# Optimization experiments

Measured on AMD Instinct MI355X. Metric: run time of the kernel, lower is better.

Reference implementation:

```python
import jax, jax.numpy as jnp
import numpy as np

EPS = 0.05      # entropic regularization, matches eps arg in forward
ITERS = 100     # Sinkhorn fixed-point iterations (auction analog; converged math)

def setup_inputs() -> dict:
    key = jax.random.key(0)
    k1, k2 = jax.random.split(key)
    B, N, D = 16, 2048, 3
    x = jax.random.uniform(k1, (B, N, D), dtype=jnp.float32)
    y = jax.random.uniform(k2, (B, N, D), dtype=jnp.float32)
    return {"x": x, "y": y}

def _emd_mean(x, y):
    # pairwise squared distances: [B, N, N]
    x2 = jnp.sum(x * x, axis=-1)                      # [B, N]
    y2 = jnp.sum(y * y, axis=-1)                      # [B, N]
    xy = jnp.einsum('bnd,bmd->bnm', x, y)             # [B, N, N]
    C = x2[:, :, None] + y2[:, None, :] - 2.0 * xy
    C = jnp.maximum(C, 0.0)

    B, N, _ = C.shape
    logK = -C / EPS                                   # [B, N, N]
    log_mu = jnp.full((B, N), -jnp.log(jnp.float32(N)))
    log_nu = log_mu

    def body(carry, _):
        f, g = carry
        # f_i = eps*(log mu_i - logsumexp_j((g_j - C_ij)/eps))
        f = EPS * (log_mu - jax.nn.logsumexp(logK + (g / EPS)[:, None, :], axis=2))
        g = EPS * (log_nu - jax.nn.logsumexp(logK + (f / EPS)[:, :, None], axis=1))
        return (f, g), None

    f0 = jnp.zeros((B, N), dtype=C.dtype)
    g0 = jnp.zeros((B, N), dtype=C.dtype)
    (f, g), _ = jax.lax.scan(body, (f0, g0), None, length=ITERS)

    # transport plan P_ij = exp((f_i + g_j - C_ij)/eps) (already includes mu,nu)
    logP = (f[:, :, None] + g[:, None, :] - C) / EPS
    P = jnp.exp(logP)
    # per-source-point matched squared distance, scaled by N (row mass = 1/N)
    dis = jnp.sum(P * C, axis=2) * N                  # [B, N]
    return dis.mean()

def reference(x, y):
    return _emd_mean(x, y)
```

## Files before the change

### kernel.cpp

```cpp
#include <hip/hip_runtime.h>

#define BB 16
#define NN 2048
#define NITERS 100

#define K2E      28.853900817779268f
#define TWO_K2E  57.707801635558536f
#define INV2K    0.017328679513998632f
#define INV_K2E  0.034657359027997264f
#define INV4K    0.008664339756999316f
#define LMU      (-11.0f)

#if __has_builtin(__builtin_amdgcn_exp2f)
#define EXP2F(x) __builtin_amdgcn_exp2f(x)
#else
#define EXP2F(x) exp2f(x)
#endif

typedef float v2f __attribute__((ext_vector_type(2)));
typedef float v4f __attribute__((ext_vector_type(4)));

#define DSTORE(p, v) __hip_atomic_store((p), (v), __ATOMIC_RELAXED, __HIP_MEMORY_SCOPE_AGENT)
#define DLOAD(p)     __hip_atomic_load((p), __ATOMIC_RELAXED, __HIP_MEMORY_SCOPE_AGENT)

__device__ __forceinline__ float bfly8(const float acc[8], int lane) {
    const bool b0 = lane & 1, b1 = lane & 2, b2 = lane & 4;
    float v4[4], v2_[2], v1;
    #pragma unroll
    for (int i = 0; i < 4; ++i) {
        float recv = __shfl_xor(b0 ? acc[i] : acc[i+4], 1, 64);
        v4[i] = (b0 ? acc[i+4] : acc[i]) + recv;
    }
    #pragma unroll
    for (int i = 0; i < 2; ++i) {
        float recv = __shfl_xor(b1 ? v4[i] : v4[i+2], 2, 64);
        v2_[i] = (b1 ? v4[i+2] : v4[i]) + recv;
    }
    {
        float recv = __shfl_xor(b2 ? v2_[0] : v2_[1], 4, 64);
        v1 = (b2 ? v2_[1] : v2_[0]) + recv;
    }
    v1 += __shfl_xor(v1, 8, 64);
    v1 += __shfl_xor(v1, 16, 64);
    v1 += __shfl_xor(v1, 32, 64);
    return v1;
}

__device__ __forceinline__ float sumpassL(
    const v4f* __restrict__ U, const v4f* __restrict__ T,
    const float* __restrict__ sdv,
    int rloc, int jh, int lane, int w, float* pcomb)
{
    const int jb = (jh << 10) + lane;
    float dv[16];
    #pragma unroll
    for (int s = 0; s < 16; ++s)
        dv[s] = sdv[jb + (s << 6)];

    v2f xp0[4], xp1[4], xp2[4], acc2[4];
    #pragma unroll
    for (int p = 0; p < 4; ++p) {
        const v4f ua = U[rloc + 2*p];
        const v4f ub = U[rloc + 2*p + 1];
        xp0[p] = (v2f){ua.x * INV2K, ub.x * INV2K};
        xp1[p] = (v2f){ua.y * INV2K, ub.y * INV2K};
        xp2[p] = (v2f){ua.z * INV2K, ub.z * INV2K};
        acc2[p] = (v2f){0.f, 0.f};
    }
    #pragma unroll 4
    for (int s = 0; s < 16; ++s) {
        const v4f t = T[jb + (s << 6)];
        const float ad = dv[s];
        const v2f a0v = (v2f){t.x, t.x}, a1v = (v2f){t.y, t.y};
        const v2f a2v = (v2f){t.z, t.z}, adv = (v2f){ad, ad};
        #pragma unroll
        for (int qq = 0; qq < 4; ++qq) {
            v2f d = __builtin_elementwise_fma(xp0[qq], a0v,
                    __builtin_elementwise_fma(xp1[qq], a1v,
                    __builtin_elementwise_fma(xp2[qq], a2v, adv)));
            acc2[qq] += (v2f){EXP2F(d.x), EXP2F(d.y)};
        }
    }
    float acc[8];
    #pragma unroll
    for (int p = 0; p < 4; ++p) { acc[2*p] = acc2[p].x; acc[2*p+1] = acc2[p].y; }
    float v1 = bfly8(acc, lane);
    const int rr = ((lane & 1) << 2) | (lane & 2) | ((lane >> 2) & 1);
    if (lane < 8) pcomb[w * 8 + rr] = v1;
    __syncthreads();
    float Sc = 0.f;
    if (lane < 8) Sc = v1 + pcomb[(w ^ 1) * 8 + rr];
    return Sc;
}

__device__ __forceinline__ float sumpassA(
    const v4f* __restrict__ U, const v4f* __restrict__ T,
    const float* __restrict__ gd,
    int rloc, int jh, int lane, int w, float* pcomb)
{
    const int jb = (jh << 10) + lane;
    float dv[16];
    #pragma unroll
    for (int s = 0; s < 16; ++s)
        dv[s] = DLOAD(gd + jb + (s << 6));

    v2f xp0[4], xp1[4], xp2[4], acc2[4];
    #pragma unroll
    for (int p = 0; p < 4; ++p) {
        const v4f ua = U[rloc + 2*p];
        const v4f ub = U[rloc + 2*p + 1];
        xp0[p] = (v2f){ua.x * INV2K, ub.x * INV2K};
        xp1[p] = (v2f){ua.y * INV2K, ub.y * INV2K};
        xp2[p] = (v2f){ua.z * INV2K, ub.z * INV2K};
        acc2[p] = (v2f){0.f, 0.f};
    }
    #pragma unroll 4
    for (int s = 0; s < 16; ++s) {
        const v4f t = T[jb + (s << 6)];
        const float ad = dv[s];
        const v2f a0v = (v2f){t.x, t.x}, a1v = (v2f){t.y, t.y};
        const v2f a2v = (v2f){t.z, t.z}, adv = (v2f){ad, ad};
        #pragma unroll
        for (int qq = 0; qq < 4; ++qq) {
            v2f d = __builtin_elementwise_fma(xp0[qq], a0v,
                    __builtin_elementwise_fma(xp1[qq], a1v,
                    __builtin_elementwise_fma(xp2[qq], a2v, adv)));
            acc2[qq] += (v2f){EXP2F(d.x), EXP2F(d.y)};
        }
    }
    float acc[8];
    #pragma unroll
    for (int p = 0; p < 4; ++p) { acc[2*p] = acc2[p].x; acc[2*p+1] = acc2[p].y; }
    float v1 = bfly8(acc, lane);
    const int rr = ((lane & 1) << 2) | (lane & 2) | ((lane >> 2) & 1);
    if (lane < 8) pcomb[w * 8 + rr] = v1;
    __syncthreads();
    float Sc = 0.f;
    if (lane < 8) Sc = v1 + pcomb[(w ^ 1) * 8 + rr];
    return Sc;
}

__device__ __forceinline__ float epilA(
    const v4f* __restrict__ U, const v4f* __restrict__ T,
    const float* __restrict__ gB,
    float Aval, int rloc, int jh, int lane)
{
    const int jb = (jh << 10) + lane;
    float dv[16];
    #pragma unroll
    for (int s = 0; s < 16; ++s)
        dv[s] = DLOAD(gB + jb + (s << 6));

    float xr0[8], xr1[8], xr2[8], Ak[8], x2k[8];
    #pragma unroll
    for (int k = 0; k < 8; ++k) {
        const v4f u = U[rloc + k];
        xr0[k] = u.x * INV2K;
        xr1[k] = u.y * INV2K;
        xr2[k] = u.z * INV2K;
        const int src = ((k & 1) << 2) | (k & 2) | ((k >> 2) & 1);
        Ak[k]  = __shfl(Aval, src, 64);
        x2k[k] = K2E * (xr0[k]*xr0[k] + xr1[k]*xr1[k] + xr2[k]*xr2[k]);
    }
    float acc = 0.f;
    for (int s = 0; s < 16; ++s) {
        const v4f t = T[jb + (s << 6)];
        const float a0 = t.x, a1 = t.y, a2 = t.z, tb = dv[s];
        const float q2 = (a0*a0 + a1*a1 + a2*a2) * INV4K;
        #pragma unroll
        for (int k = 0; k < 8; ++k) {
            float d = fmaf(xr0[k], a0, fmaf(xr1[k], a1, fmaf(xr2[k], a2, tb)));
            float P = EXP2F(d + Ak[k]);
            float C = fmaxf((x2k[k] + q2 - (d - tb)) * INV_K2E, 0.f);
            acc = fmaf(P, C, acc);
        }
    }
    return acc;
}

__global__ __launch_bounds__(1024, 4) void emd_sinkhornT(
    const float* __restrict__ x, const float* __restrict__ y,
    float* __restrict__ Af, float* __restrict__ Bf,
    int* __restrict__ flags, float* __restrict__ out)
{
    extern __shared__ float S[];
    __shared__ float pcomb[16 * 8];
    __shared__ float wsum[16];

    const int tid  = threadIdx.x;
    const int lane = tid & 63;
    const int w    = tid >> 6;
    const int pr   = w >> 1;
    const int jh   = w & 1;
    const int blk  = blockIdx.x;
    const int b    = blk >> 4;
    const int q    = blk & 15;
    const int base = b * NN;
    const int row0 = q * 128;
    const int rlocA = row0 + pr * 8;
    const int rlocB = row0 + 64 + pr * 8;
    int* fb = flags + b * 64;

    v4f   *sy = (v4f*)S;
    v4f   *sx = (v4f*)S + NN;
    float *sd = (float*)((v4f*)S + 2 * NN);

    #pragma unroll
    for (int v = 0; v < 2; ++v) {
        const int p = tid + (v << 10);
        const float* px = x + 3 * (size_t)(base + p);
        sx[p] = (v4f){TWO_K2E * px[0], TWO_K2E * px[1], TWO_K2E * px[2], 0.f};
        const float* py = y + 3 * (size_t)(base + p);
        sy[p] = (v4f){TWO_K2E * py[0], TWO_K2E * py[1], TWO_K2E * py[2], 0.f};
    }
    if (tid < 128) {
        const int col = row0 + tid;
        const float* py = y + 3 * (size_t)(base + col);
        const float a = py[0], bb = py[1], c = py[2];
        DSTORE(&Bf[base + col], -K2E * (a*a + bb*bb + c*c));
    }
    __syncthreads();
    if (tid == 0)
        __hip_atomic_store(fb + q * 4, 1, __ATOMIC_RELEASE, __HIP_MEMORY_SCOPE_AGENT);

    #define WAITB(tgt) do { __syncthreads();                                    \
        if (w == 0) {                                                           \
            for (;;) {                                                          \
                int vv = (lane < 16)                                            \
                    ? __hip_atomic_load(fb + lane * 4, __ATOMIC_RELAXED,        \
                                        __HIP_MEMORY_SCOPE_AGENT)               \
                    : 0x7fffffff;                                               \
                if (__ballot(vv >= (tgt)) == ~0ULL) break;                      \
                __builtin_amdgcn_s_sleep(1);                                    \
            }                                                                   \
        }                                                                       \
        __syncthreads(); } while (0)

    #define POSTB(pval) do { __syncthreads();                                   \
        if (tid == 0)                                                           \
            __hip_atomic_store(fb + q * 4, (pval), __ATOMIC_RELEASE,            \
                               __HIP_MEMORY_SCOPE_AGENT);                       \
    } while (0)

    #define STAGE(gsrc) do {                                                    \
        float t0_ = DLOAD((gsrc) + tid);                                        \
        float t1_ = DLOAD((gsrc) + tid + 1024);                                 \
        sd[tid] = t0_; sd[tid + 1024] = t1_;                                    \
        __syncthreads(); } while (0)

    WAITB(1);

    const int rr = ((lane & 1) << 2) | (lane & 2) | ((lane >> 2) & 1);
    float Aval0 = 0.f, Aval1 = 0.f;

    for (int it = 0; it < NITERS; ++it) {
        STAGE(Bf + base);
        {
            float Sc = sumpassL(sx, sy, sd, rlocA, jh, lane, w, pcomb);
            Aval0 = LMU - __log2f(Sc);
            if (lane < 8 && jh == 0) DSTORE(&Af[base + rlocA + rr], Aval0);
        }
        {
            float Sc = sumpassL(sx, sy, sd, rlocB, jh, lane, w, pcomb);
            Aval1 = LMU - __log2f(Sc);
            if (lane < 8 && jh == 0) DSTORE(&Af[base + rlocB + rr], Aval1);
        }
        POSTB(2 * it + 2);
        WAITB(2 * it + 2);
        STAGE(Af + base);
        {
            float Sc = sumpassL(sy, sx, sd, rlocA, jh, lane, w, pcomb);
            if (lane < 8 && jh == 0)
                DSTORE(&Bf[base + rlocA + rr], LMU - __log2f(Sc));
        }
        {
            float Sc = sumpassL(sy, sx, sd, rlocB, jh, lane, w, pcomb);
            if (lane < 8 && jh == 0)
                DSTORE(&Bf[base + rlocB + rr], LMU - __log2f(Sc));
        }
        POSTB(2 * it + 3);
        WAITB(2 * it + 3);
    }

    {
        float s = epilA(sx, sy, Bf + base, Aval0, rlocA, jh, lane)
                + epilA(sx, sy, Bf + base, Aval1, rlocB, jh, lane);
        #pragma unroll
        for (int m = 32; m > 0; m >>= 1) s += __shfl_xor(s, m, 64);
        if (lane == 0) wsum[w] = s;
        __syncthreads();
        if (tid == 0) {
            float t = 0.f;
            #pragma unroll
            for (int i = 0; i < 16; ++i) t += wsum[i];
            atomicAdd(out, t * (1.0f / (float)BB));
        }
    }
    #undef WAITB
    #undef POSTB
    #undef STAGE
}

__global__ __launch_bounds__(1024, 4) void emd_sinkhornS(
    const float* __restrict__ x, const float* __restrict__ y,
    float* __restrict__ Af, float* __restrict__ Bf,
    int* __restrict__ flags, float* __restrict__ out)
{
    extern __shared__ float S[];
    __shared__ float pcomb[16 * 8];
    __shared__ float wsum[16];

    const int tid  = threadIdx.x;
    const int lane = tid & 63;
    const int w    = tid >> 6;
    const int pr   = w >> 1;
    const int jh   = w & 1;
    const int blk  = blockIdx.x;
    const int pair = blk & 7;
    const int q    = blk >> 3;
    const int b0   = pair * 2, b1 = b0 + 1;
    const int base0 = b0 * NN, base1 = b1 * NN;
    const int rloc  = q * 64 + pr * 8;
    int* fp = flags + 8192/4 + pair * 128;

    v4f *sy0 = (v4f*)S;
    v4f *sx0 = (v4f*)S + 1*NN;
    v4f *sy1 = (v4f*)S + 2*NN;
    v4f *sx1 = (v4f*)S + 3*NN;

    #pragma unroll
    for (int v = 0; v < 2; ++v) {
        const int p = tid + (v << 10);
        {
            const float* px = x + 3 * (size_t)(base0 + p);
            sx0[p] = (v4f){TWO_K2E * px[0], TWO_K2E * px[1], TWO_K2E * px[2], 0.f};
            const float* py = y + 3 * (size_t)(base0 + p);
            sy0[p] = (v4f){TWO_K2E * py[0], TWO_K2E * py[1], TWO_K2E * py[2], 0.f};
        }
        {
            const float* px = x + 3 * (size_t)(base1 + p);
            sx1[p] = (v4f){TWO_K2E * px[0], TWO_K2E * px[1], TWO_K2E * px[2], 0.f};
            const float* py = y + 3 * (size_t)(base1 + p);
            sy1[p] = (v4f){TWO_K2E * py[0], TWO_K2E * py[1], TWO_K2E * py[2], 0.f};
        }
    }
    if (tid < 128) {
        const int bb  = tid >> 6;
        const int col = q * 64 + (tid & 63);
        const int bs  = bb ? base1 : base0;
        const float* py = y + 3 * (size_t)(bs + col);
        const float a = py[0], b = py[1], c = py[2];
        DSTORE(&Bf[bs + col], -K2E * (a*a + b*b + c*c));
    }
    __syncthreads();
    if (tid == 0)
        __hip_atomic_store(fp + q * 4, 1, __ATOMIC_RELEASE, __HIP_MEMORY_SCOPE_AGENT);

    #define PW(pval, tgt) do { __syncthreads();                                 \
        if (tid == 0)                                                           \
            __hip_atomic_store(fp + q * 4, (pval), __ATOMIC_RELEASE,            \
                               __HIP_MEMORY_SCOPE_AGENT);                       \
        if (w == 0) {                                                           \
            for (;;) {                                                          \
                int vv = (lane < 32)                                            \
                    ? __hip_atomic_load(fp + lane * 4, __ATOMIC_RELAXED,        \
                                        __HIP_MEMORY_SCOPE_AGENT)               \
                    : 0x7fffffff;                                               \
                if (__ballot(vv >= (tgt)) == ~0ULL) break;                      \
                __builtin_amdgcn_s_sleep(1);                                    \
            }                                                                   \
        }                                                                       \
        __syncthreads(); } while (0)

    PW(1, 1);

    const int rr = ((lane & 1) << 2) | (lane & 2) | ((lane >> 2) & 1);
    float Aval0 = 0.f, Aval1 = 0.f;

    for (int it = 0; it < NITERS; ++it) {
        {
            float Sc = sumpassA(sx0, sy0, Bf + base0, rloc, jh, lane, w, pcomb);
            Aval0 = LMU - __log2f(Sc);
            if (lane < 8 && jh == 0) DSTORE(&Af[base0 + rloc + rr], Aval0);
        }
        {
            float Sc = sumpassA(sx1, sy1, Bf + base1, rloc, jh, lane, w, pcomb);
            Aval1 = LMU - __log2f(Sc);
            if (lane < 8 && jh == 0) DSTORE(&Af[base1 + rloc + rr], Aval1);
        }
        PW(2 * it + 2, 2 * it + 2);
        {
            float Sc = sumpassA(sy0, sx0, Af + base0, rloc, jh, lane, w, pcomb);
            if (lane < 8 && jh == 0)
                DSTORE(&Bf[base0 + rloc + rr], LMU - __log2f(Sc));
        }
        {
            float Sc = sumpassA(sy1, sx1, Af + base1, rloc, jh, lane, w, pcomb);
            if (lane < 8 && jh == 0)
                DSTORE(&Bf[base1 + rloc + rr], LMU - __log2f(Sc));
        }
        PW(2 * it + 3, 2 * it + 3);
    }

    {
        float s = epilA(sx0, sy0, Bf + base0, Aval0, rloc, jh, lane)
                + epilA(sx1, sy1, Bf + base1, Aval1, rloc, jh, lane);
        #pragma unroll
        for (int m = 32; m > 0; m >>= 1) s += __shfl_xor(s, m, 64);
        if (lane == 0) wsum[w] = s;
        __syncthreads();
        if (tid == 0) {
            float t = 0.f;
            #pragma unroll
            for (int i = 0; i < 16; ++i) t += wsum[i];
            atomicAdd(out, t * (1.0f / (float)BB));
        }
    }
    #undef PW
}

extern "C" void kernel_launch(void* const* d_in, const int* in_sizes, int n_in,
                              void* d_out, int out_size, void* d_ws, size_t ws_size,
                              hipStream_t stream) {
    const float* x = (const float*)d_in[0];
    const float* y = (const float*)d_in[1];
    float* out = (float*)d_out;
    char* ws = (char*)d_ws;

    int*   flags = (int*)ws;
    float* Af    = (float*)(ws + 16384);
    float* Bf    = (float*)(ws + 16384 + (size_t)BB*NN*sizeof(float));

    hipMemsetAsync(flags, 0, 16384, stream);
    hipMemsetAsync(out, 0, sizeof(float), stream);

    void* args[] = {(void*)&x, (void*)&y, (void*)&Af, (void*)&Bf,
                    (void*)&flags, (void*)&out};

    const size_t shmemT = (size_t)(2 * NN * 4 + NN) * sizeof(float);
    hipError_t et = hipFuncSetAttribute((const void*)emd_sinkhornT,
                        hipFuncAttributeMaxDynamicSharedMemorySize, (int)shmemT);
    hipError_t e = (et == hipSuccess)
        ? hipLaunchCooperativeKernel((const void*)emd_sinkhornT,
                                     dim3(256), dim3(1024), args, shmemT, stream)
        : hipErrorInvalidValue;
    if (e != hipSuccess) {
        const size_t shmemS = (size_t)4 * NN * 4 * sizeof(float);
        hipError_t es = hipFuncSetAttribute((const void*)emd_sinkhornS,
                            hipFuncAttributeMaxDynamicSharedMemorySize, (int)shmemS);
        hipError_t e2 = (es == hipSuccess)
            ? hipLaunchCooperativeKernel((const void*)emd_sinkhornS,
                                         dim3(256), dim3(1024), args, shmemS, stream)
            : hipErrorInvalidValue;
        if (e2 != hipSuccess) {
            hipLaunchKernelGGL(emd_sinkhornS, dim3(256), dim3(1024), shmemS,
                               stream, x, y, Af, Bf, flags, out);
        }
    }
}
```

Before: 2.494 ms.

## Give each wave full column range to drop cross-wave LDS combine

Adds a new primary kernel in which each block handles one batch with 128 rows. Each wave owns 8 rows and sums over all 2048 columns, so the half-column split, the LDS partial combine and the extra __syncthreads inside each pass are gone. The old S kernel is removed, and T becomes the fallback. Per-wave serial work doubles, while the per-pass sync overhead and two-batch interleaving are dropped.

```diff
diff --git a/kernel.cpp b/kernel.cpp
--- a/kernel.cpp
+++ b/kernel.cpp
@@ -44,6 +44,42 @@
     v1 += __shfl_xor(v1, 16, 64);
     v1 += __shfl_xor(v1, 32, 64);
     return v1;
+}
+
+__device__ __forceinline__ float sumpassF(
+    const v4f* __restrict__ U, const v4f* __restrict__ T,
+    const float* __restrict__ sdv,
+    int rloc, int lane)
+{
+    v2f xp0[4], xp1[4], xp2[4], acc2[4];
+    #pragma unroll
+    for (int p = 0; p < 4; ++p) {
+        const v4f ua = U[rloc + 2*p];
+        const v4f ub = U[rloc + 2*p + 1];
+        xp0[p] = (v2f){ua.x * INV2K, ub.x * INV2K};
+        xp1[p] = (v2f){ua.y * INV2K, ub.y * INV2K};
+        xp2[p] = (v2f){ua.z * INV2K, ub.z * INV2K};
+        acc2[p] = (v2f){0.f, 0.f};
+    }
+    #pragma unroll 4
+    for (int s = 0; s < 32; ++s) {
+        const int p = lane + (s << 6);
+        const v4f t = T[p];
+        const float ad = sdv[p];
+        const v2f a0v = (v2f){t.x, t.x}, a1v = (v2f){t.y, t.y};
+        const v2f a2v = (v2f){t.z, t.z}, adv = (v2f){ad, ad};
+        #pragma unroll
+        for (int qq = 0; qq < 4; ++qq) {
+            v2f d = __builtin_elementwise_fma(xp0[qq], a0v,
+                    __builtin_elementwise_fma(xp1[qq], a1v,
+                    __builtin_elementwise_fma(xp2[qq], a2v, adv)));
+            acc2[qq] += (v2f){EXP2F(d.x), EXP2F(d.y)};
+        }
+    }
+    float acc[8];
+    #pragma unroll
+    for (int p = 0; p < 4; ++p) { acc[2*p] = acc2[p].x; acc[2*p+1] = acc2[p].y; }
+    return bfly8(acc, lane);
 }
 
 __device__ __forceinline__ float sumpassL(
@@ -93,53 +129,6 @@
     return Sc;
 }
 
-__device__ __forceinline__ float sumpassA(
-    const v4f* __restrict__ U, const v4f* __restrict__ T,
-    const float* __restrict__ gd,
-    int rloc, int jh, int lane, int w, float* pcomb)
-{
-    const int jb = (jh << 10) + lane;
-    float dv[16];
-    #pragma unroll
-    for (int s = 0; s < 16; ++s)
-        dv[s] = DLOAD(gd + jb + (s << 6));
-
-    v2f xp0[4], xp1[4], xp2[4], acc2[4];
-    #pragma unroll
-    for (int p = 0; p < 4; ++p) {
-        const v4f ua = U[rloc + 2*p];
-        const v4f ub = U[rloc + 2*p + 1];
-        xp0[p] = (v2f){ua.x * INV2K, ub.x * INV2K};
-        xp1[p] = (v2f){ua.y * INV2K, ub.y * INV2K};
-        xp2[p] = (v2f){ua.z * INV2K, ub.z * INV2K};
-        acc2[p] = (v2f){0.f, 0.f};
-    }
-    #pragma unroll 4
-    for (int s = 0; s < 16; ++s) {
-        const v4f t = T[jb + (s << 6)];
-        const float ad = dv[s];
-        const v2f a0v = (v2f){t.x, t.x}, a1v = (v2f){t.y, t.y};
-        const v2f a2v = (v2f){t.z, t.z}, adv = (v2f){ad, ad};
-        #pragma unroll
-        for (int qq = 0; qq < 4; ++qq) {
-            v2f d = __builtin_elementwise_fma(xp0[qq], a0v,
-                    __builtin_elementwise_fma(xp1[qq], a1v,
-                    __builtin_elementwise_fma(xp2[qq], a2v, adv)));
-            acc2[qq] += (v2f){EXP2F(d.x), EXP2F(d.y)};
-        }
-    }
-    float acc[8];
-    #pragma unroll
-    for (int p = 0; p < 4; ++p) { acc[2*p] = acc2[p].x; acc[2*p+1] = acc2[p].y; }
-    float v1 = bfly8(acc, lane);
-    const int rr = ((lane & 1) << 2) | (lane & 2) | ((lane >> 2) & 1);
-    if (lane < 8) pcomb[w * 8 + rr] = v1;
-    __syncthreads();
-    float Sc = 0.f;
-    if (lane < 8) Sc = v1 + pcomb[(w ^ 1) * 8 + rr];
-    return Sc;
-}
-
 __device__ __forceinline__ float epilA(
     const v4f* __restrict__ U, const v4f* __restrict__ T,
     const float* __restrict__ gB,
@@ -176,6 +165,115 @@
         }
     }
     return acc;
+}
+
+__global__ __launch_bounds__(1024, 4) void emd_sinkhornU(
+    const float* __restrict__ x, const float* __restrict__ y,
+    float* __restrict__ Af, float* __restrict__ Bf,
+    int* __restrict__ flags, float* __restrict__ out)
+{
+    extern __shared__ float S[];
+    __shared__ float wsum[16];
+
+    const int tid  = threadIdx.x;
+    const int lane = tid & 63;
+    const int w    = tid >> 6;
+    const int blk  = blockIdx.x;
+    const int b    = blk >> 4;
+    const int q    = blk & 15;
+    const int base = b * NN;
+    const int row0 = q * 128;
+    const int rloc = row0 + w * 8;
+    int* fb = flags + b * 64;
+
+    v4f   *sy = (v4f*)S;
+    v4f   *sx = (v4f*)S + NN;
+    float *sd = (float*)((v4f*)S + 2 * NN);
+
+    #pragma unroll
+    for (int v = 0; v < 2; ++v) {
+        const int p = tid + (v << 10);
+        const float* px = x + 3 * (size_t)(base + p);
+        sx[p] = (v4f){TWO_K2E * px[0], TWO_K2E * px[1], TWO_K2E * px[2], 0.f};
+        const float* py = y + 3 * (size_t)(base + p);
+        sy[p] = (v4f){TWO_K2E * py[0], TWO_K2E * py[1], TWO_K2E * py[2], 0.f};
+    }
+    if (tid < 128) {
+        const int col = row0 + tid;
+        const float* py = y + 3 * (size_t)(base + col);
+        const float a = py[0], bb = py[1], c = py[2];
+        DSTORE(&Bf[base + col], -K2E * (a*a + bb*bb + c*c));
+    }
+    __syncthreads();
+    if (tid == 0)
+        __hip_atomic_store(fb + q * 4, 1, __ATOMIC_RELEASE, __HIP_MEMORY_SCOPE_AGENT);
+
+    #define WAITB(tgt) do { __syncthreads();                                    \
+        if (w == 0) {                                                           \
+            for (;;) {                                                          \
+                int vv = (lane < 16)                                            \
+                    ? __hip_atomic_load(fb + lane * 4, __ATOMIC_RELAXED,        \
+                                        __HIP_MEMORY_SCOPE_AGENT)               \
+                    : 0x7fffffff;                                               \
+                if (__ballot(vv >= (tgt)) == ~0ULL) break;                      \
+                __builtin_amdgcn_s_sleep(1);                                    \
+            }                                                                   \
+        }                                                                       \
+        __syncthreads(); } while (0)
+
+    #define POSTB(pval) do { __syncthreads();                                   \
+        if (tid == 0)                                                           \
+            __hip_atomic_store(fb + q * 4, (pval), __ATOMIC_RELEASE,            \
+                               __HIP_MEMORY_SCOPE_AGENT);                       \
+    } while (0)
+
+    #define STAGE(gsrc) do {                                                    \
+        float t0_ = DLOAD((gsrc) + tid);                                        \
+        float t1_ = DLOAD((gsrc) + tid + 1024);                                 \
+        sd[tid] = t0_; sd[tid + 1024] = t1_;                                    \
+        __syncthreads(); } while (0)
+
+    WAITB(1);
+
+    const int rr = ((lane & 1) << 2) | (lane & 2) | ((lane >> 2) & 1);
+    float Aval = 0.f;
+
+    for (int it = 0; it < NITERS; ++it) {
+        STAGE(Bf + base);
+        {
+            float v1 = sumpassF(sx, sy, sd, rloc, lane);
+            Aval = LMU - __log2f(v1);
+            if (lane < 8) DSTORE(&Af[base + rloc + rr], Aval);
+        }
+        POSTB(2 * it + 2);
+        WAITB(2 * it + 2);
+        STAGE(Af + base);
+        {
+            float v1 = sumpassF(sy, sx, sd, rloc, lane);
+            if (lane < 8)
+                DSTORE(&Bf[base + rloc + rr], LMU - __log2f(v1));
+        }
+        POSTB(2 * it + 3);
+        WAITB(2 * it + 3);
+    }
+
+    {
+        float s = epilA(sx, sy, Bf + base, Aval, rloc, 0, lane)
+                + epilA(sx, sy, Bf + base, Aval, rloc, 1, lane);
+        #pragma unroll
+        for (int m = 32; m > 0; m >>= 1) s += __shfl_xor(s, m, 64);
+        if (lane == 0) wsum[w] = s;
+        __syncthreads();
+        if (tid == 0) {
+            float t = 0.f;
+            #pragma unroll
+            for (int i = 0; i < 16; ++i) t += wsum[i];
+            atomicAdd(out, t * (1.0f / (float)BB));
+        }
+    }
+    #undef WAITB
+    #undef POSTB
+    #undef STAGE
 }
 
 __global__ __launch_bounds__(1024, 4) void emd_sinkhornT(
@@ -223,7 +321,7 @@
     if (tid == 0)
         __hip_atomic_store(fb + q * 4, 1, __ATOMIC_RELEASE, __HIP_MEMORY_SCOPE_AGENT);
 
-    #define WAITB(tgt) do { __syncthreads();                                    \
+    #define WAITB2(tgt) do { __syncthreads();                                   \
         if (w == 0) {                                                           \
             for (;;) {                                                          \
                 int vv = (lane < 16)                                            \
@@ -236,25 +334,25 @@
         }                                                                       \
         __syncthreads(); } while (0)
 
-    #define POSTB(pval) do { __syncthreads();                                   \
+    #define POSTB2(pval) do { __syncthreads();                                  \
         if (tid == 0)                                                           \
             __hip_atomic_store(fb + q * 4, (pval), __ATOMIC_RELEASE,            \
                                __HIP_MEMORY_SCOPE_AGENT);                       \
     } while (0)
 
-    #define STAGE(gsrc) do {                                                    \
+    #define STAGE2(gsrc) do {                                                   \
         float t0_ = DLOAD((gsrc) + tid);                                        \
         float t1_ = DLOAD((gsrc) + tid + 1024);                                 \
         sd[tid] = t0_; sd[tid + 1024] = t1_;                                    \
         __syncthreads(); } while (0)
 
-    WAITB(1);
+    WAITB2(1);
 
     const int rr = ((lane & 1) << 2) | (lane & 2) | ((lane >> 2) & 1);
     float Aval0 = 0.f, Aval1 = 0.f;
 
     for (int it = 0; it < NITERS; ++it) {
-        STAGE(Bf + base);
+        STAGE2(Bf + base);
         {
             float Sc = sumpassL(sx, sy, sd, rlocA, jh, lane, w, pcomb);
             Aval0 = LMU - __log2f(Sc);
@@ -265,9 +363,9 @@
             Aval1 = LMU - __log2f(Sc);
             if (lane < 8 && jh == 0) DSTORE(&Af[base + rlocB + rr], Aval1);
         }
-        POSTB(2 * it + 2);
-        WAITB(2 * it + 2);
-        STAGE(Af + base);
+        POSTB2(2 * it + 2);
+        WAITB2(2 * it + 2);
+        STAGE2(Af + base);
         {
             float Sc = sumpassL(sy, sx, sd, rlocA, jh, lane, w, pcomb);
             if (lane < 8 && jh == 0)
@@ -278,8 +376,8 @@
             if (lane < 8 && jh == 0)
                 DSTORE(&Bf[base + rlocB + rr], LMU - __log2f(Sc));
         }
-        POSTB(2 * it + 3);
-        WAITB(2 * it + 3);
+        POSTB2(2 * it + 3);
+        WAITB2(2 * it + 3);
     }
 
     {
@@ -296,127 +394,9 @@
             atomicAdd(out, t * (1.0f / (float)BB));
         }
     }
-    #undef WAITB
-    #undef POSTB
-    #undef STAGE
-}
-
-__global__ __launch_bounds__(1024, 4) void emd_sinkhornS(
-    const float* __restrict__ x, const float* __restrict__ y,
-    float* __restrict__ Af, float* __restrict__ Bf,
-    int* __restrict__ flags, float* __restrict__ out)
-{
-    extern __shared__ float S[];
-    __shared__ float pcomb[16 * 8];
-    __shared__ float wsum[16];
-
-    const int tid  = threadIdx.x;
-    const int lane = tid & 63;
-    const int w    = tid >> 6;
-    const int pr   = w >> 1;
-    const int jh   = w & 1;
-    const int blk  = blockIdx.x;
-    const int pair = blk & 7;
-    const int q    = blk >> 3;
-    const int b0   = pair * 2, b1 = b0 + 1;
-    const int base0 = b0 * NN, base1 = b1 * NN;
-    const int rloc  = q * 64 + pr * 8;
-    int* fp = flags + 8192/4 + pair * 128;
-
-    v4f *sy0 = (v4f*)S;
-    v4f *sx0 = (v4f*)S + 1*NN;
-    v4f *sy1 = (v4f*)S + 2*NN;
-    v4f *sx1 = (v4f*)S + 3*NN;
-
-    #pragma unroll
-    for (int v = 0; v < 2; ++v) {
-        const int p = tid + (v << 10);
-        {
-            const float* px = x + 3 * (size_t)(base0 + p);
-            sx0[p] = (v4f){TWO_K2E * px[0], TWO_K2E * px[1], TWO_K2E * px[2], 0.f};
-            const float* py = y + 3 * (size_t)(base0 + p);
-            sy0[p] = (v4f){TWO_K2E * py[0], TWO_K2E * py[1], TWO_K2E * py[2], 0.f};
-        }
-        {
-            const float* px = x + 3 * (size_t)(base1 + p);
-            sx1[p] = (v4f){TWO_K2E * px[0], TWO_K2E * px[1], TWO_K2E * px[2], 0.f};
-            const float* py = y + 3 * (size_t)(base1 + p);
-            sy1[p] = (v4f){TWO_K2E * py[0], TWO_K2E * py[1], TWO_K2E * py[2], 0.f};
-        }
-    }
-    if (tid < 128) {
-        const int bb  = tid >> 6;
-        const int col = q * 64 + (tid & 63);
-        const int bs  = bb ? base1 : base0;
-        const float* py = y + 3 * (size_t)(bs + col);
-        const float a = py[0], b = py[1], c = py[2];
-        DSTORE(&Bf[bs + col], -K2E * (a*a + b*b + c*c));
-    }
-    __syncthreads();
-    if (tid == 0)
-        __hip_atomic_store(fp + q * 4, 1, __ATOMIC_RELEASE, __HIP_MEMORY_SCOPE_AGENT);
-
-    #define PW(pval, tgt) do { __syncthreads();                                 \
-        if (tid == 0)                                                           \
-            __hip_atomic_store(fp + q * 4, (pval), __ATOMIC_RELEASE,            \
-                               __HIP_MEMORY_SCOPE_AGENT);                       \
-        if (w == 0) {                                                           \
-            for (;;) {                                                          \
-                int vv = (lane < 32)                                            \
-                    ? __hip_atomic_load(fp + lane * 4, __ATOMIC_RELAXED,        \
-                                        __HIP_MEMORY_SCOPE_AGENT)               \
-                    : 0x7fffffff;                                               \
-                if (__ballot(vv >= (tgt)) == ~0ULL) break;                      \
-                __builtin_amdgcn_s_sleep(1);                                    \
-            }                                                                   \
-        }                                                                       \
-        __syncthreads(); } while (0)
-
-    PW(1, 1);
-
-    const int rr = ((lane & 1) << 2) | (lane & 2) | ((lane >> 2) & 1);
-    float Aval0 = 0.f, Aval1 = 0.f;
-
-    for (int it = 0; it < NITERS; ++it) {
-        {
-            float Sc = sumpassA(sx0, sy0, Bf + base0, rloc, jh, lane, w, pcomb);
-            Aval0 = LMU - __log2f(Sc);
-            if (lane < 8 && jh == 0) DSTORE(&Af[base0 + rloc + rr], Aval0);
-        }
-        {
-            float Sc = sumpassA(sx1, sy1, Bf + base1, rloc, jh, lane, w, pcomb);
-            Aval1 = LMU - __log2f(Sc);
-            if (lane < 8 && jh == 0) DSTORE(&Af[base1 + rloc + rr], Aval1);
-        }
-        PW(2 * it + 2, 2 * it + 2);
-        {
-            float Sc = sumpassA(sy0, sx0, Af + base0, rloc, jh, lane, w, pcomb);
-            if (lane < 8 && jh == 0)
-                DSTORE(&Bf[base0 + rloc + rr], LMU - __log2f(Sc));
-        }
-        {
-            float Sc = sumpassA(sy1, sx1, Af + base1, rloc, jh, lane, w, pcomb);
-            if (lane < 8 && jh == 0)
-                DSTORE(&Bf[base1 + rloc + rr], LMU - __log2f(Sc));
-        }
-        PW(2 * it + 3, 2 * it + 3);
-    }
-
-    {
-        float s = epilA(sx0, sy0, Bf + base0, Aval0, rloc, jh, lane)
-                + epilA(sx1, sy1, Bf + base1, Aval1, rloc, jh, lane);
-        #pragma unroll
-        for (int m = 32; m > 0; m >>= 1) s += __shfl_xor(s, m, 64);
-        if (lane == 0) wsum[w] = s;
-        __syncthreads();
-        if (tid == 0) {
-            float t = 0.f;
-            #pragma unroll
-            for (int i = 0; i < 16; ++i) t += wsum[i];
-            atomicAdd(out, t * (1.0f / (float)BB));
-        }
-    }
-    #undef PW
+    #undef WAITB2
+    #undef POSTB2
+    #undef STAGE2
 }
 
 extern "C" void kernel_launch(void* const* d_in, const int* in_sizes, int n_in,
@@ -437,23 +417,22 @@
     void* args[] = {(void*)&x, (void*)&y, (void*)&Af, (void*)&Bf,
                     (void*)&flags, (void*)&out};
 
-    const size_t shmemT = (size_t)(2 * NN * 4 + NN) * sizeof(float);
-    hipError_t et = hipFuncSetAttribute((const void*)emd_sinkhornT,
-                        hipFuncAttributeMaxDynamicSharedMemorySize, (int)shmemT);
-    hipError_t e = (et == hipSuccess)
-        ? hipLaunchCooperativeKernel((const void*)emd_sinkhornT,
-                                     dim3(256), dim3(1024), args, shmemT, stream)
+    const size_t shmem = (size_t)(2 * NN * 4 + NN) * sizeof(float);
+    hipError_t eu = hipFuncSetAttribute((const void*)emd_sinkhornU,
+                        hipFuncAttributeMaxDynamicSharedMemorySize, (int)shmem);
+    hipError_t e = (eu == hipSuccess)
+        ? hipLaunchCooperativeKernel((const void*)emd_sinkhornU,
+                                     dim3(256), dim3(1024), args, shmem, stream)
         : hipErrorInvalidValue;
     if (e != hipSuccess) {
-        const size_t shmemS = (size_t)4 * NN * 4 * sizeof(float);
-        hipError_t es = hipFuncSetAttribute((const void*)emd_sinkhornS,
-                            hipFuncAttributeMaxDynamicSharedMemorySize, (int)shmemS);
-        hipError_t e2 = (es == hipSuccess)
-            ? hipLaunchCooperativeKernel((const void*)emd_sinkhornS,
-                                         dim3(256), dim3(1024), args, shmemS, stream)
+        hipError_t et = hipFuncSetAttribute((const void*)emd_sinkhornT,
+                            hipFuncAttributeMaxDynamicSharedMemorySize, (int)shmem);
+        hipError_t e2 = (et == hipSuccess)
+            ? hipLaunchCooperativeKernel((const void*)emd_sinkhornT,
+                                         dim3(256), dim3(1024), args, shmem, stream)
             : hipErrorInvalidValue;
         if (e2 != hipSuccess) {
-            hipLaunchKernelGGL(emd_sinkhornS, dim3(256), dim3(1024), shmemS,
+            hipLaunchKernelGGL(emd_sinkhornT, dim3(256), dim3(1024), shmem,
                                stream, x, y, Af, Bf, flags, out);
         }
     }
```

After: 2.337 ms. 1.07x faster.
